# Kernel optimization log

Measured on AMD Instinct MI355X. Metric: run time of the kernel, lower is better.

## Reference

```python
import jax, jax.numpy as jnp
import numpy as np

N = 10000      # nodes
E = 160000     # edges
F_IN = 128     # input_feature
G = 64         # graphs in batch
NC = 10        # num_classes
H1, H2, H3 = 1000, 700, 200


def _xavier(k, fi, fo):
    lim = float(np.sqrt(6.0 / (fi + fo)))
    return jax.random.uniform(k, (fi, fo), jnp.float32, -lim, lim)


def setup_inputs() -> dict:
    key = jax.random.key(0)
    ks = jax.random.split(key, 8)
    x = jax.random.normal(ks[0], (N, F_IN), jnp.float32)
    edge_index = jax.random.randint(ks[1], (2, E), 0, N)
    batch = jnp.sort(jax.random.randint(ks[2], (N,), 0, G))
    return {
        "x": x,
        "edge_index": edge_index,
        "batch": batch,
        "W1": _xavier(ks[3], F_IN, H1), "b1": jnp.zeros((H1,), jnp.float32),
        "W2": _xavier(ks[4], H1, H2),   "b2": jnp.zeros((H2,), jnp.float32),
        "W3": _xavier(ks[5], H2, H3),   "b3": jnp.zeros((H3,), jnp.float32),
        "Wl": _xavier(ks[6], H3, NC),   "bl": jnp.zeros((NC,), jnp.float32),
    }


def _gcn_conv(x, W, b, src, dst, dinv):
    # GCNConv: h = xW; out_i = sum_{j->i} d_j^-1/2 d_i^-1/2 h_j + d_i^-1 h_i + b
    h = x @ W
    coef = dinv[src] * dinv[dst]                      # [E]
    agg = jax.ops.segment_sum(h[src] * coef[:, None], dst, num_segments=N)
    agg = agg + h * (dinv * dinv)[:, None]            # self-loop term
    return agg + b


def reference(x, edge_index, batch, W1, b1, W2, b2, W3, b3, Wl, bl):
    src, dst = edge_index[0], edge_index[1]
    # degree with self-loops (edge weight 1), computed on target nodes
    deg = jax.ops.segment_sum(jnp.ones((E,), x.dtype), dst, num_segments=N) + 1.0
    dinv = jax.lax.rsqrt(deg)

    h = jax.nn.relu(_gcn_conv(x, W1, b1, src, dst, dinv))
    h = jax.nn.relu(_gcn_conv(h, W2, b2, src, dst, dinv))
    h = jax.nn.relu(_gcn_conv(h, W3, b3, src, dst, dinv))

    # global_mean_pool over graph ids
    s = jax.ops.segment_sum(h, batch, num_segments=G)
    cnt = jax.ops.segment_sum(jnp.ones((N,), h.dtype), batch, num_segments=G)
    pooled = s / jnp.maximum(cnt, 1.0)[:, None]

    # dropout is identity in eval mode
    return pooled @ Wl + bl
```

## Files before the change

kernel.cpp:

```cpp
#include <hip/hip_runtime.h>
#include <hip/hip_bf16.h>
#include <stdint.h>


#define SLOT 64

__device__ __forceinline__ uint16_t f2b(float f) {
    union { float f; uint32_t u; } v; v.f = f;
    return (uint16_t)((v.u + 0x7fffu + ((v.u >> 16) & 1u)) >> 16);
}
__device__ __forceinline__ float blo(uint32_t u) { union { uint32_t u; float f; } v; v.u = u << 16; return v.f; }
__device__ __forceinline__ float bhi(uint32_t u) { union { uint32_t u; float f; } v; v.u = u & 0xffff0000u; return v.f; }

__global__ void k_prep(const float* __restrict__ W1, const float* __restrict__ W2,
                       const float* __restrict__ W3,
                       uint16_t* __restrict__ T1, uint16_t* __restrict__ T2,
                       uint16_t* __restrict__ T3,
                       const float* __restrict__ b1, const float* __restrict__ b2,
                       const float* __restrict__ b3,
                       float* __restrict__ p1, float* __restrict__ p2,
                       float* __restrict__ p3,
                       const int* __restrict__ src, const int* __restrict__ dst,
                       int* __restrict__ cursor, int* __restrict__ slots,
                       float* __restrict__ outz, int outn,
                       int E, int N, int F, int H1, int H2, int H3,
                       int Fp, int H1p, int H2p, int H3p) {
    __shared__ float tile[32][33];
    int z = blockIdx.z;
    if (z < 3) {
        const float* W; uint16_t* T; int K, Nn, Kp, Np;
        if (z == 0)      { W = W1; T = T1; K = F;  Nn = H1; Kp = Fp;  Np = H1p; }
        else if (z == 1) { W = W2; T = T2; K = H1; Nn = H2; Kp = H1p; Np = H2p; }
        else             { W = W3; T = T3; K = H2; Nn = H3; Kp = H2p; Np = H3p; }
        if ((int)blockIdx.x * 32 >= Kp || (int)blockIdx.y * 32 >= Np) return;
        int k0 = blockIdx.x * 32, n0 = blockIdx.y * 32;
        int tx = threadIdx.x, ty = threadIdx.y;
        for (int i = ty; i < 32; i += 8) {
            int k = k0 + i, n = n0 + tx;
            tile[i][tx] = (k < K && n < Nn) ? W[(size_t)k * Nn + n] : 0.f;
        }
        __syncthreads();
        for (int i = ty; i < 32; i += 8) {
            int n = n0 + i, k = k0 + tx;
            T[(size_t)n * Kp + k] = f2b(tile[tx][i]);
        }
    } else if (z == 3) {
        int id = (blockIdx.y * gridDim.x + blockIdx.x) * 256 + threadIdx.y * 32 + threadIdx.x;
        if (id < H1p) p1[id] = (id < H1) ? b1[id] : 0.f;
        else if (id < H1p + H2p) { int k = id - H1p; p2[k] = (k < H2) ? b2[k] : 0.f; }
        else if (id < H1p + H2p + H3p) { int k = id - H1p - H2p; p3[k] = (k < H3) ? b3[k] : 0.f; }
        if (id < outn) outz[id] = 0.f;
    } else {
        int fb = blockIdx.y * gridDim.x + blockIdx.x;
        int g = fb & 7, b = fb >> 3;
        int seg = (N + 7) >> 3;
        int lo = g * seg;
        int hi = lo + seg; if (hi > N) hi = N;
        int per = (E + 127) >> 7;
        int e0 = b * per;
        int e1 = e0 + per; if (e1 > E) e1 = E;
        int tid = threadIdx.y * 32 + threadIdx.x;
        for (int e = e0 + tid; e < e1; e += 256) {
            int d = dst[e];
            if (d >= lo && d < hi) {
                int s = src[e];
                int pos = atomicAdd(&cursor[d], 1);
                if (pos < SLOT) slots[d * SLOT + pos] = s;
            }
        }
    }
}

__global__ __launch_bounds__(256) void k_agg_x(
    const float* __restrict__ x, uint16_t* __restrict__ out,
    const int* __restrict__ deg_, const int* __restrict__ slots,
    int N, int F4, int pc) {
    int seg = blockIdx.x & 7;
    int segLen = (N + 7) >> 3;
    int wave = threadIdx.x >> 6, lane = threadIdx.x & 63;
    int half = lane >> 5, sub = lane & 31;
    int item = (blockIdx.x >> 3) * 128 + wave * 32 + sub;
    int rel = item / pc;
    if (rel >= segLen) return;
    int node = seg * segLen + rel;
    if (node >= N) return;
    int j = item - rel * pc;
    int degN = deg_[node];
    float dv = rsqrtf((float)degN + 1.0f);
    int deg = degN > SLOT ? SLOT : degN;
    int base = node * SLOT;
    const float4* x4 = (const float4*)x;
    float a[8] = {0.f, 0.f, 0.f, 0.f, 0.f, 0.f, 0.f, 0.f};
    if (half == 0) {
        float4 xl = x4[(size_t)node * F4 + 2 * j];
        float4 xh = x4[(size_t)node * F4 + 2 * j + 1];
        a[0] = dv * xl.x; a[1] = dv * xl.y; a[2] = dv * xl.z; a[3] = dv * xl.w;
        a[4] = dv * xh.x; a[5] = dv * xh.y; a[6] = dv * xh.z; a[7] = dv * xh.w;
    }
    int D8 = deg & ~7;
    for (int e = 4 * half; e < D8; e += 8) {
        int4 q = *(const int4*)&slots[base + e];
        float c0 = rsqrtf((float)deg_[q.x] + 1.0f);
        float c1 = rsqrtf((float)deg_[q.y] + 1.0f);
        float c2 = rsqrtf((float)deg_[q.z] + 1.0f);
        float c3 = rsqrtf((float)deg_[q.w] + 1.0f);
        float4 l0 = x4[(size_t)q.x * F4 + 2 * j], h0 = x4[(size_t)q.x * F4 + 2 * j + 1];
        float4 l1 = x4[(size_t)q.y * F4 + 2 * j], h1 = x4[(size_t)q.y * F4 + 2 * j + 1];
        float4 l2 = x4[(size_t)q.z * F4 + 2 * j], h2 = x4[(size_t)q.z * F4 + 2 * j + 1];
        float4 l3 = x4[(size_t)q.w * F4 + 2 * j], h3 = x4[(size_t)q.w * F4 + 2 * j + 1];
        a[0] += c0 * l0.x; a[1] += c0 * l0.y; a[2] += c0 * l0.z; a[3] += c0 * l0.w;
        a[4] += c0 * h0.x; a[5] += c0 * h0.y; a[6] += c0 * h0.z; a[7] += c0 * h0.w;
        a[0] += c1 * l1.x; a[1] += c1 * l1.y; a[2] += c1 * l1.z; a[3] += c1 * l1.w;
        a[4] += c1 * h1.x; a[5] += c1 * h1.y; a[6] += c1 * h1.z; a[7] += c1 * h1.w;
        a[0] += c2 * l2.x; a[1] += c2 * l2.y; a[2] += c2 * l2.z; a[3] += c2 * l2.w;
        a[4] += c2 * h2.x; a[5] += c2 * h2.y; a[6] += c2 * h2.z; a[7] += c2 * h2.w;
        a[0] += c3 * l3.x; a[1] += c3 * l3.y; a[2] += c3 * l3.z; a[3] += c3 * l3.w;
        a[4] += c3 * h3.x; a[5] += c3 * h3.y; a[6] += c3 * h3.z; a[7] += c3 * h3.w;
    }
    int t0 = half ? (D8 + 4 < deg ? D8 + 4 : deg) : D8;
    int t1 = half ? deg : (D8 + 4 < deg ? D8 + 4 : deg);
    for (int e = t0; e < t1; ++e) {
        int s = slots[base + e];
        float c = rsqrtf((float)deg_[s] + 1.0f);
        float4 l = x4[(size_t)s * F4 + 2 * j], h = x4[(size_t)s * F4 + 2 * j + 1];
        a[0] += c * l.x; a[1] += c * l.y; a[2] += c * l.z; a[3] += c * l.w;
        a[4] += c * h.x; a[5] += c * h.y; a[6] += c * h.z; a[7] += c * h.w;
    }
#pragma unroll
    for (int t = 0; t < 8; ++t) a[t] += __shfl_xor(a[t], 32, 64);
    if (half == 0) {
#pragma unroll
        for (int t = 0; t < 8; ++t) a[t] *= dv;
        uint4 o;
        o.x = (uint32_t)f2b(a[0]) | ((uint32_t)f2b(a[1]) << 16);
        o.y = (uint32_t)f2b(a[2]) | ((uint32_t)f2b(a[3]) << 16);
        o.z = (uint32_t)f2b(a[4]) | ((uint32_t)f2b(a[5]) << 16);
        o.w = (uint32_t)f2b(a[6]) | ((uint32_t)f2b(a[7]) << 16);
        ((uint4*)out)[(size_t)node * (F4 >> 1) + j] = o;
    }
}

__global__ __launch_bounds__(256) void k_agg_panel(
    const uint16_t* __restrict__ in, uint16_t* __restrict__ out,
    const int* __restrict__ deg_, const int* __restrict__ slots,
    const float* __restrict__ bias,
    int N, int Hc, int pc, int P, int relu) {
    int slotg = blockIdx.x & 7;
    int panel = slotg % P;
    int seg   = slotg / P;
    int nseg  = 8 / P;
    int segLen = (N + nseg - 1) / nseg;
    int wave = threadIdx.x >> 6, lane = threadIdx.x & 63;
    int half = lane >> 5, sub = lane & 31;
    int item = (blockIdx.x >> 3) * 128 + wave * 32 + sub;
    int rel = item / pc;
    if (rel >= segLen) return;
    int node = seg * segLen + rel;
    if (node >= N) return;
    int j = panel * pc + (item - rel * pc);
    int deg = deg_[node];
    float dv = rsqrtf((float)deg + 1.0f);
    if (deg > SLOT) deg = SLOT;
    int base = node * SLOT;
    const uint4* in4 = (const uint4*)in;
    float a[8] = {0.f, 0.f, 0.f, 0.f, 0.f, 0.f, 0.f, 0.f};
    if (half == 0) {
        uint4 v = in4[(size_t)node * Hc + j];
        a[0] = blo(v.x); a[1] = bhi(v.x);
        a[2] = blo(v.y); a[3] = bhi(v.y);
        a[4] = blo(v.z); a[5] = bhi(v.z);
        a[6] = blo(v.w); a[7] = bhi(v.w);
    }
    int D8 = deg & ~7;
    int e = 4 * half;
    if (e < D8) {
        int4 q = *(const int4*)&slots[base + e];
        uint4 h0 = in4[(size_t)q.x * Hc + j];
        uint4 h1 = in4[(size_t)q.y * Hc + j];
        uint4 h2 = in4[(size_t)q.z * Hc + j];
        uint4 h3 = in4[(size_t)q.w * Hc + j];
        for (e += 8; e < D8; e += 8) {
            int4 qn = *(const int4*)&slots[base + e];
            uint4 g0 = in4[(size_t)qn.x * Hc + j];
            uint4 g1 = in4[(size_t)qn.y * Hc + j];
            uint4 g2 = in4[(size_t)qn.z * Hc + j];
            uint4 g3 = in4[(size_t)qn.w * Hc + j];
            a[0] += blo(h0.x); a[1] += bhi(h0.x);
            a[2] += blo(h0.y); a[3] += bhi(h0.y);
            a[4] += blo(h0.z); a[5] += bhi(h0.z);
            a[6] += blo(h0.w); a[7] += bhi(h0.w);
            a[0] += blo(h1.x); a[1] += bhi(h1.x);
            a[2] += blo(h1.y); a[3] += bhi(h1.y);
            a[4] += blo(h1.z); a[5] += bhi(h1.z);
            a[6] += blo(h1.w); a[7] += bhi(h1.w);
            a[0] += blo(h2.x); a[1] += bhi(h2.x);
            a[2] += blo(h2.y); a[3] += bhi(h2.y);
            a[4] += blo(h2.z); a[5] += bhi(h2.z);
            a[6] += blo(h2.w); a[7] += bhi(h2.w);
            a[0] += blo(h3.x); a[1] += bhi(h3.x);
            a[2] += blo(h3.y); a[3] += bhi(h3.y);
            a[4] += blo(h3.z); a[5] += bhi(h3.z);
            a[6] += blo(h3.w); a[7] += bhi(h3.w);
            h0 = g0; h1 = g1; h2 = g2; h3 = g3;
        }
        a[0] += blo(h0.x); a[1] += bhi(h0.x);
        a[2] += blo(h0.y); a[3] += bhi(h0.y);
        a[4] += blo(h0.z); a[5] += bhi(h0.z);
        a[6] += blo(h0.w); a[7] += bhi(h0.w);
        a[0] += blo(h1.x); a[1] += bhi(h1.x);
        a[2] += blo(h1.y); a[3] += bhi(h1.y);
        a[4] += blo(h1.z); a[5] += bhi(h1.z);
        a[6] += blo(h1.w); a[7] += bhi(h1.w);
        a[0] += blo(h2.x); a[1] += bhi(h2.x);
        a[2] += blo(h2.y); a[3] += bhi(h2.y);
        a[4] += blo(h2.z); a[5] += bhi(h2.z);
        a[6] += blo(h2.w); a[7] += bhi(h2.w);
        a[0] += blo(h3.x); a[1] += bhi(h3.x);
        a[2] += blo(h3.y); a[3] += bhi(h3.y);
        a[4] += blo(h3.z); a[5] += bhi(h3.z);
        a[6] += blo(h3.w); a[7] += bhi(h3.w);
    }
    int t0 = half ? (D8 + 4 < deg ? D8 + 4 : deg) : D8;
    int t1 = half ? deg : (D8 + 4 < deg ? D8 + 4 : deg);
    for (int ee = t0; ee < t1; ++ee) {
        int s0 = slots[base + ee];
        uint4 h = in4[(size_t)s0 * Hc + j];
        a[0] += blo(h.x); a[1] += bhi(h.x);
        a[2] += blo(h.y); a[3] += bhi(h.y);
        a[4] += blo(h.z); a[5] += bhi(h.z);
        a[6] += blo(h.w); a[7] += bhi(h.w);
    }
#pragma unroll
    for (int t = 0; t < 8; ++t) a[t] += __shfl_xor(a[t], 32, 64);
    if (half == 0) {
        if (bias) {
            const float4* b4 = (const float4*)bias;
            float4 b0 = b4[2 * j], b1 = b4[2 * j + 1];
            a[0] = fmaf(a[0], dv, b0.x); a[1] = fmaf(a[1], dv, b0.y);
            a[2] = fmaf(a[2], dv, b0.z); a[3] = fmaf(a[3], dv, b0.w);
            a[4] = fmaf(a[4], dv, b1.x); a[5] = fmaf(a[5], dv, b1.y);
            a[6] = fmaf(a[6], dv, b1.z); a[7] = fmaf(a[7], dv, b1.w);
        } else {
#pragma unroll
            for (int t = 0; t < 8; ++t) a[t] *= dv;
        }
        if (relu) {
#pragma unroll
            for (int t = 0; t < 8; ++t) a[t] = fmaxf(a[t], 0.f);
        }
        uint4 o;
        o.x = (uint32_t)f2b(a[0]) | ((uint32_t)f2b(a[1]) << 16);
        o.y = (uint32_t)f2b(a[2]) | ((uint32_t)f2b(a[3]) << 16);
        o.z = (uint32_t)f2b(a[4]) | ((uint32_t)f2b(a[5]) << 16);
        o.w = (uint32_t)f2b(a[6]) | ((uint32_t)f2b(a[7]) << 16);
        ((uint4*)out)[(size_t)node * Hc + j] = o;
    }
}

__global__ __launch_bounds__(256) void k_pool_cls4(
    const uint16_t* __restrict__ h, const int* __restrict__ batch,
    const float* __restrict__ Wl, const float* __restrict__ bl,
    float* __restrict__ out, int N, int H, int Hc, int NC) {
    __shared__ float part[8][26][8];
    __shared__ float pooled[200];
    int g = blockIdx.x >> 2, b = blockIdx.x & 3;
    int tid = threadIdx.x;
    int lo = 0, hi = N;
    while (lo < hi) { int m = (lo + hi) >> 1; if (batch[m] < g) lo = m + 1; else hi = m; }
    int start = lo; hi = N;
    while (lo < hi) { int m = (lo + hi) >> 1; if (batch[m] < g + 1) lo = m + 1; else hi = m; }
    int end = lo;
    int j = tid & 31, s = tid >> 5;
    int jmax = H >> 3;
    const uint4* h4 = (const uint4*)h;
    if (j < jmax) {
        float a[8] = {0.f, 0.f, 0.f, 0.f, 0.f, 0.f, 0.f, 0.f};
        for (int node = start + s * 4 + b; node < end; node += 32) {
            uint4 v = h4[(size_t)node * Hc + j];
            a[0] += blo(v.x); a[1] += bhi(v.x);
            a[2] += blo(v.y); a[3] += bhi(v.y);
            a[4] += blo(v.z); a[5] += bhi(v.z);
            a[6] += blo(v.w); a[7] += bhi(v.w);
        }
#pragma unroll
        for (int t = 0; t < 8; ++t) part[s][j][t] = a[t];
    }
    __syncthreads();
    if (tid < H) {
        float sum = 0.f;
#pragma unroll
        for (int ss = 0; ss < 8; ++ss) sum += part[ss][tid >> 3][tid & 7];
        pooled[tid] = sum;
    }
    __syncthreads();
    if (tid < 64) {
        float scale = 1.0f / fmaxf((float)(end - start), 1.0f);
        int c = tid & 15, q = tid >> 4;
        float acc = 0.f;
        if (c < NC) {
            for (int k = q; k < H; k += 4)
                acc += pooled[k] * Wl[(size_t)k * NC + c];
        }
        acc += __shfl_xor(acc, 16, 64);
        acc += __shfl_xor(acc, 32, 64);
        if (q == 0 && c < NC) {
            float v = acc * scale;
            if (b == 0) v += bl[c];
            atomicAdd(&out[(size_t)g * NC + c], v);
        }
    }
}

typedef __attribute__((ext_vector_type(8))) short short8;
typedef __attribute__((ext_vector_type(4))) float floatx4;

#define LDSP(p) ((__attribute__((address_space(3))) void*)(uintptr_t)(p))
#define GLBP(p) ((const __attribute__((address_space(1))) void*)(uintptr_t)(p))

__global__ __launch_bounds__(256) void k_gemm128(
    const uint16_t* __restrict__ A, const uint16_t* __restrict__ Bt,
    const float* __restrict__ bias, uint16_t* __restrict__ Cout,
    int M, int Kp, int Np, int relu, int nrg, int nr,
    const int* __restrict__ degp) {
    int bid = blockIdx.x;
    int rsub = bid & 7;
    int t_ = bid >> 3;
    int rg = t_ % nrg, cc = t_ / nrg;
    int rt = rg * 8 + rsub;
    if (rt >= nr) return;
    int row0 = rt * 128, col0 = cc * 128;

    __shared__ uint16_t As[128 * 64];
    __shared__ uint16_t Bs[128 * 64];
    int tid = threadIdx.x;
    int wave = tid >> 6, lane = tid & 63;
    int quad = lane >> 4, m16 = lane & 15;
    int wr = wave >> 1, wc = wave & 1;

    int rA = tid >> 3;
    int cA = (tid & 7) ^ (rA & 7);
    const uint16_t* gA = A  + (size_t)(row0 + rA) * Kp + cA * 8;
    const uint16_t* gB = Bt + (size_t)(col0 + rA) * Kp + cA * 8;
    uint16_t* lA = As + tid * 8;
    uint16_t* lB = Bs + tid * 8;
    size_t rowStep32 = (size_t)32 * Kp;

    floatx4 acc[4][4];
#pragma unroll
    for (int i = 0; i < 4; ++i)
#pragma unroll
        for (int j = 0; j < 4; ++j) acc[i][j] = (floatx4){0.f, 0.f, 0.f, 0.f};

    const short* Ash = (const short*)As;
    const short* Bsh = (const short*)Bs;
    int swA = m16 & 7;

    for (int k0 = 0; k0 < Kp; k0 += 64) {
#pragma unroll
        for (int p = 0; p < 4; ++p) {
            __builtin_amdgcn_global_load_lds(GLBP(gA + p * rowStep32), LDSP(lA + p * 2048), 16, 0, 0);
            __builtin_amdgcn_global_load_lds(GLBP(gB + p * rowStep32), LDSP(lB + p * 2048), 16, 0, 0);
        }
        gA += 64; gB += 64;
        __syncthreads();
#pragma unroll
        for (int h = 0; h < 2; ++h) {
            short8 af[4], bf[4];
            int c = h * 4 + quad;
            int pos = (c ^ swA) * 8;
#pragma unroll
            for (int i = 0; i < 4; ++i)
                af[i] = *(const short8*)&Ash[(wr * 64 + i * 16 + m16) * 64 + pos];
#pragma unroll
            for (int j = 0; j < 4; ++j)
                bf[j] = *(const short8*)&Bsh[(wc * 64 + j * 16 + m16) * 64 + pos];
#pragma unroll
            for (int i = 0; i < 4; ++i)
#pragma unroll
                for (int j = 0; j < 4; ++j)
                    acc[i][j] = __builtin_amdgcn_mfma_f32_16x16x32_bf16(af[i], bf[j], acc[i][j], 0, 0, 0);
        }
        __syncthreads();
    }

    float bv[4];
#pragma unroll
    for (int j = 0; j < 4; ++j) {
        int n = col0 + wc * 64 + j * 16 + m16;
        bv[j] = bias ? bias[n] : 0.f;
    }
#pragma unroll
    for (int i = 0; i < 4; ++i) {
        int mBase = row0 + wr * 64 + i * 16 + quad * 4;
#pragma unroll
        for (int r = 0; r < 4; ++r) {
            int m = mBase + r;
            if (m < M) {
                float s = degp ? rsqrtf((float)degp[m] + 1.0f) : 1.f;
#pragma unroll
                for (int j = 0; j < 4; ++j) {
                    int n = col0 + wc * 64 + j * 16 + m16;
                    float v = acc[i][j][r] * s + bv[j];
                    if (relu) v = fmaxf(v, 0.f);
                    Cout[(size_t)m * Np + n] = f2b(v);
                }
            }
        }
    }
}

__global__ __launch_bounds__(256) void k_gemm64(
    const uint16_t* __restrict__ A, const uint16_t* __restrict__ Bt,
    const float* __restrict__ bias, uint16_t* __restrict__ Cout,
    int M, int Kp, int Np, int relu, int nrg, int nr,
    const int* __restrict__ degp) {
    int bid = blockIdx.x;
    int rsub = bid & 7;
    int t_ = bid >> 3;
    int rg = t_ % nrg, cc = t_ / nrg;
    int rt = rg * 8 + rsub;
    if (rt >= nr) return;
    int row0 = rt * 128, col0 = cc * 64;

    __shared__ uint16_t As[128 * 64];
    __shared__ uint16_t Bs[64 * 64];
    int tid = threadIdx.x;
    int wave = tid >> 6, lane = tid & 63;
    int quad = lane >> 4, m16 = lane & 15;
    int wr = wave >> 1, wc = wave & 1;

    int rA = tid >> 3;
    int cA = (tid & 7) ^ (rA & 7);
    const uint16_t* gA = A  + (size_t)(row0 + rA) * Kp + cA * 8;
    const uint16_t* gB = Bt + (size_t)(col0 + rA) * Kp + cA * 8;
    uint16_t* lA = As + tid * 8;
    uint16_t* lB = Bs + tid * 8;
    size_t rowStep32 = (size_t)32 * Kp;

    floatx4 acc[4][2];
#pragma unroll
    for (int i = 0; i < 4; ++i)
#pragma unroll
        for (int j = 0; j < 2; ++j) acc[i][j] = (floatx4){0.f, 0.f, 0.f, 0.f};

    const short* Ash = (const short*)As;
    const short* Bsh = (const short*)Bs;
    int swA = m16 & 7;

    for (int k0 = 0; k0 < Kp; k0 += 64) {
#pragma unroll
        for (int p = 0; p < 4; ++p)
            __builtin_amdgcn_global_load_lds(GLBP(gA + p * rowStep32), LDSP(lA + p * 2048), 16, 0, 0);
#pragma unroll
        for (int p = 0; p < 2; ++p)
            __builtin_amdgcn_global_load_lds(GLBP(gB + p * rowStep32), LDSP(lB + p * 2048), 16, 0, 0);
        gA += 64; gB += 64;
        __syncthreads();
#pragma unroll
        for (int h = 0; h < 2; ++h) {
            short8 af[4], bf[2];
            int c = h * 4 + quad;
            int pos = (c ^ swA) * 8;
#pragma unroll
            for (int i = 0; i < 4; ++i)
                af[i] = *(const short8*)&Ash[(wr * 64 + i * 16 + m16) * 64 + pos];
#pragma unroll
            for (int j = 0; j < 2; ++j)
                bf[j] = *(const short8*)&Bsh[(wc * 32 + j * 16 + m16) * 64 + pos];
#pragma unroll
            for (int i = 0; i < 4; ++i)
#pragma unroll
                for (int j = 0; j < 2; ++j)
                    acc[i][j] = __builtin_amdgcn_mfma_f32_16x16x32_bf16(af[i], bf[j], acc[i][j], 0, 0, 0);
        }
        __syncthreads();
    }

    float bv[2];
#pragma unroll
    for (int j = 0; j < 2; ++j) {
        int n = col0 + wc * 32 + j * 16 + m16;
        bv[j] = bias ? bias[n] : 0.f;
    }
#pragma unroll
    for (int i = 0; i < 4; ++i) {
        int mBase = row0 + wr * 64 + i * 16 + quad * 4;
#pragma unroll
        for (int r = 0; r < 4; ++r) {
            int m = mBase + r;
            if (m < M) {
                float s = degp ? rsqrtf((float)degp[m] + 1.0f) : 1.f;
#pragma unroll
                for (int j = 0; j < 2; ++j) {
                    int n = col0 + wc * 32 + j * 16 + m16;
                    float v = acc[i][j][r] * s + bv[j];
                    if (relu) v = fmaxf(v, 0.f);
                    Cout[(size_t)m * Np + n] = f2b(v);
                }
            }
        }
    }
}

static inline size_t align256(size_t x) { return (x + 255) & ~(size_t)255; }
static inline int pad128(int x) { return (x + 127) & ~127; }

extern "C" void kernel_launch(void* const* d_in, const int* in_sizes, int n_in,
                              void* d_out, int out_size, void* d_ws, size_t ws_size,
                              hipStream_t stream) {
    const float* x   = (const float*)d_in[0];
    const int*   ei  = (const int*)d_in[1];
    const int*   bat = (const int*)d_in[2];
    const float* W1  = (const float*)d_in[3];
    const float* b1  = (const float*)d_in[4];
    const float* W2  = (const float*)d_in[5];
    const float* b2  = (const float*)d_in[6];
    const float* W3  = (const float*)d_in[7];
    const float* b3  = (const float*)d_in[8];
    const float* Wl  = (const float*)d_in[9];
    const float* bl  = (const float*)d_in[10];

    const int N  = in_sizes[2];
    const int E  = in_sizes[1] / 2;
    const int F  = in_sizes[0] / N;
    const int H1 = in_sizes[4];
    const int H2 = in_sizes[6];
    const int H3 = in_sizes[8];
    const int NC = in_sizes[10];
    const int* src = ei;
    const int* dst = ei + E;

    const int Mp  = pad128(N);
    const int Fp  = F;
    const int H1p = pad128(H1);
    const int H2p = pad128(H2);
    const int H3p = pad128(H3);

    char* p = (char*)d_ws;
    size_t off = 0;
    auto carve = [&](size_t bytes) { void* q = p + off; off += align256(bytes); return q; };
    uint16_t* bufA   = (uint16_t*)carve((size_t)Mp * 2048);
    uint16_t* bufB   = (uint16_t*)carve((size_t)Mp * 2048);
    uint16_t* W1t    = (uint16_t*)carve((size_t)H1p * Fp * 2);
    uint16_t* W2t    = (uint16_t*)carve((size_t)H2p * H1p * 2);
    uint16_t* W3t    = (uint16_t*)carve((size_t)H3p * H2p * 2);
    float* b1p       = (float*)carve((size_t)H1p * 4);
    float* b2p       = (float*)carve((size_t)H2p * 4);
    float* b3p       = (float*)carve((size_t)H3p * 4);
    int*   cursor    = (int*)carve((size_t)N * 4);
    int*   slots     = (int*)carve((size_t)N * SLOT * 4);
    (void)ws_size;

    hipMemsetAsync(cursor, 0, (size_t)N * 4, stream);

    k_prep<<<dim3(32, 32, 5), dim3(32, 8), 0, stream>>>(
        W1, W2, W3, W1t, W2t, W3t, b1, b2, b3, b1p, b2p, b3p,
        src, dst, cursor, slots, (float*)d_out, out_size,
        E, N, F, H1, H2, H3, Fp, H1p, H2p, H3p);

    auto agg_grid = [&](int P, int pc) {
        int nseg = 8 / P;
        int segLen = (N + nseg - 1) / nseg;
        return 8 * ((segLen * pc + 127) / 128);
    };

    const int nr  = Mp / 128;
    const int nrg = (nr + 7) / 8;

    k_agg_x<<<agg_grid(1, F / 8), 256, 0, stream>>>(
        x, bufA, cursor, slots, N, F / 4, F / 8);
    k_gemm128<<<nrg * 8 * (H1p / 128), 256, 0, stream>>>(
        bufA, W1t, b1p, bufB, N, Fp, H1p, 1, nrg, nr, nullptr);

    k_gemm128<<<nrg * 8 * (H2p / 128), 256, 0, stream>>>(
        bufB, W2t, nullptr, bufA, N, H1p, H2p, 0, nrg, nr, cursor);
    k_agg_panel<<<agg_grid(8, 11), 256, 0, stream>>>(
        bufA, bufB, cursor, slots, b2p, N, 96, 11, 8, 1);

    k_gemm64<<<nrg * 8 * (H3p / 64), 256, 0, stream>>>(
        bufB, W3t, nullptr, bufA, N, H2p, H3p, 0, nrg, nr, cursor);
    k_agg_panel<<<agg_grid(4, 7), 256, 0, stream>>>(
        bufA, bufB, cursor, slots, b3p, N, 32, 7, 4, 1);

    k_pool_cls4<<<64 * 4, 256, 0, stream>>>(
        (const uint16_t*)bufB, bat, Wl, bl, (float*)d_out, N, H3, H3p >> 3, NC);
}
```

Baseline: 226.4 us.

## Build edge slots with shared-memory cursors, pre-cast x to bf16, pipeline gather loop

The edge-binning stage now uses 64 blocks, each owning a node range and counting in shared-memory cursors before writing them to global memory. This removes the separate memset and the global atomics, but every block now scans the full dst array. The input features are converted to bf16 inside the prep kernel, so the first aggregation gathers half as many bytes. The aggregation loop is also software-pipelined so the next neighbor rows load while the current ones accumulate. The full-array scan per block may make the binning stage long-latency and limit its parallelism.

```diff
diff --git a/kernel.cpp b/kernel.cpp
--- a/kernel.cpp
+++ b/kernel.cpp
@@ -20,12 +20,14 @@
                        const float* __restrict__ b3,
                        float* __restrict__ p1, float* __restrict__ p2,
                        float* __restrict__ p3,
+                       const float* __restrict__ x, uint16_t* __restrict__ xbu,
                        const int* __restrict__ src, const int* __restrict__ dst,
                        int* __restrict__ cursor, int* __restrict__ slots,
                        float* __restrict__ outz, int outn,
                        int E, int N, int F, int H1, int H2, int H3,
-                       int Fp, int H1p, int H2p, int H3p) {
+                       int Fp, int H1p, int H2p, int H3p, int n8) {
     __shared__ float tile[32][33];
+    __shared__ int lcur[160];
     int z = blockIdx.z;
     if (z < 3) {
         const float* W; uint16_t* T; int K, Nn, Kp, Np;
@@ -50,31 +52,64 @@
         else if (id < H1p + H2p) { int k = id - H1p; p2[k] = (k < H2) ? b2[k] : 0.f; }
         else if (id < H1p + H2p + H3p) { int k = id - H1p - H2p; p3[k] = (k < H3) ? b3[k] : 0.f; }
         if (id < outn) outz[id] = 0.f;
+        if (id < n8) {
+            const float4* x4 = (const float4*)x;
+            float4 a = x4[2 * id], b = x4[2 * id + 1];
+            uint4 o;
+            o.x = (uint32_t)f2b(a.x) | ((uint32_t)f2b(a.y) << 16);
+            o.y = (uint32_t)f2b(a.z) | ((uint32_t)f2b(a.w) << 16);
+            o.z = (uint32_t)f2b(b.x) | ((uint32_t)f2b(b.y) << 16);
+            o.w = (uint32_t)f2b(b.z) | ((uint32_t)f2b(b.w) << 16);
+            ((uint4*)xbu)[id] = o;
+        }
     } else {
         int fb = blockIdx.y * gridDim.x + blockIdx.x;
-        int g = fb & 7, b = fb >> 3;
-        int seg = (N + 7) >> 3;
-        int lo = g * seg;
+        if (fb >= 64) return;
+        int seg = (N + 63) >> 6;
+        int lo = fb * seg;
         int hi = lo + seg; if (hi > N) hi = N;
-        int per = (E + 127) >> 7;
-        int e0 = b * per;
-        int e1 = e0 + per; if (e1 > E) e1 = E;
         int tid = threadIdx.y * 32 + threadIdx.x;
-        for (int e = e0 + tid; e < e1; e += 256) {
+        for (int i = tid; i < seg; i += 256) lcur[i] = 0;
+        __syncthreads();
+        const int4* dst4 = (const int4*)dst;
+        int E4 = E >> 2;
+        for (int i = tid; i < E4; i += 256) {
+            int4 d4 = dst4[i];
+            int e = 4 * i;
+            if (d4.x >= lo && d4.x < hi) {
+                int pos = atomicAdd(&lcur[d4.x - lo], 1);
+                if (pos < SLOT) slots[d4.x * SLOT + pos] = src[e];
+            }
+            if (d4.y >= lo && d4.y < hi) {
+                int pos = atomicAdd(&lcur[d4.y - lo], 1);
+                if (pos < SLOT) slots[d4.y * SLOT + pos] = src[e + 1];
+            }
+            if (d4.z >= lo && d4.z < hi) {
+                int pos = atomicAdd(&lcur[d4.z - lo], 1);
+                if (pos < SLOT) slots[d4.z * SLOT + pos] = src[e + 2];
+            }
+            if (d4.w >= lo && d4.w < hi) {
+                int pos = atomicAdd(&lcur[d4.w - lo], 1);
+                if (pos < SLOT) slots[d4.w * SLOT + pos] = src[e + 3];
+            }
+        }
+        for (int e = (E4 << 2) + tid; e < E; e += 256) {
             int d = dst[e];
             if (d >= lo && d < hi) {
-                int s = src[e];
-                int pos = atomicAdd(&cursor[d], 1);
-                if (pos < SLOT) slots[d * SLOT + pos] = s;
+                int pos = atomicAdd(&lcur[d - lo], 1);
+                if (pos < SLOT) slots[d * SLOT + pos] = src[e];
             }
         }
+        __syncthreads();
+        for (int i = tid; i < seg; i += 256)
+            if (lo + i < N) cursor[lo + i] = lcur[i];
     }
 }
 
 __global__ __launch_bounds__(256) void k_agg_x(
-    const float* __restrict__ x, uint16_t* __restrict__ out,
+    const uint16_t* __restrict__ in, uint16_t* __restrict__ out,
     const int* __restrict__ deg_, const int* __restrict__ slots,
-    int N, int F4, int pc) {
+    int N, int Hc, int pc) {
     int seg = blockIdx.x & 7;
     int segLen = (N + 7) >> 3;
     int wave = threadIdx.x >> 6, lane = threadIdx.x & 63;
@@ -89,42 +124,83 @@
     float dv = rsqrtf((float)degN + 1.0f);
     int deg = degN > SLOT ? SLOT : degN;
     int base = node * SLOT;
-    const float4* x4 = (const float4*)x;
+    const uint4* in4 = (const uint4*)in;
     float a[8] = {0.f, 0.f, 0.f, 0.f, 0.f, 0.f, 0.f, 0.f};
     if (half == 0) {
-        float4 xl = x4[(size_t)node * F4 + 2 * j];
-        float4 xh = x4[(size_t)node * F4 + 2 * j + 1];
-        a[0] = dv * xl.x; a[1] = dv * xl.y; a[2] = dv * xl.z; a[3] = dv * xl.w;
-        a[4] = dv * xh.x; a[5] = dv * xh.y; a[6] = dv * xh.z; a[7] = dv * xh.w;
+        uint4 v = in4[(size_t)node * Hc + j];
+        a[0] = dv * blo(v.x); a[1] = dv * bhi(v.x);
+        a[2] = dv * blo(v.y); a[3] = dv * bhi(v.y);
+        a[4] = dv * blo(v.z); a[5] = dv * bhi(v.z);
+        a[6] = dv * blo(v.w); a[7] = dv * bhi(v.w);
     }
     int D8 = deg & ~7;
-    for (int e = 4 * half; e < D8; e += 8) {
+    int e = 4 * half;
+    if (e < D8) {
         int4 q = *(const int4*)&slots[base + e];
+        uint4 h0 = in4[(size_t)q.x * Hc + j];
+        uint4 h1 = in4[(size_t)q.y * Hc + j];
+        uint4 h2 = in4[(size_t)q.z * Hc + j];
+        uint4 h3 = in4[(size_t)q.w * Hc + j];
         float c0 = rsqrtf((float)deg_[q.x] + 1.0f);
         float c1 = rsqrtf((float)deg_[q.y] + 1.0f);
         float c2 = rsqrtf((float)deg_[q.z] + 1.0f);
         float c3 = rsqrtf((float)deg_[q.w] + 1.0f);
-        float4 l0 = x4[(size_t)q.x * F4 + 2 * j], h0 = x4[(size_t)q.x * F4 + 2 * j + 1];
-        float4 l1 = x4[(size_t)q.y * F4 + 2 * j], h1 = x4[(size_t)q.y * F4 + 2 * j + 1];
-        float4 l2 = x4[(size_t)q.z * F4 + 2 * j], h2 = x4[(size_t)q.z * F4 + 2 * j + 1];
-        float4 l3 = x4[(size_t)q.w * F4 + 2 * j], h3 = x4[(size_t)q.w * F4 + 2 * j + 1];
-        a[0] += c0 * l0.x; a[1] += c0 * l0.y; a[2] += c0 * l0.z; a[3] += c0 * l0.w;
-        a[4] += c0 * h0.x; a[5] += c0 * h0.y; a[6] += c0 * h0.z; a[7] += c0 * h0.w;
-        a[0] += c1 * l1.x; a[1] += c1 * l1.y; a[2] += c1 * l1.z; a[3] += c1 * l1.w;
-        a[4] += c1 * h1.x; a[5] += c1 * h1.y; a[6] += c1 * h1.z; a[7] += c1 * h1.w;
-        a[0] += c2 * l2.x; a[1] += c2 * l2.y; a[2] += c2 * l2.z; a[3] += c2 * l2.w;
-        a[4] += c2 * h2.x; a[5] += c2 * h2.y; a[6] += c2 * h2.z; a[7] += c2 * h2.w;
-        a[0] += c3 * l3.x; a[1] += c3 * l3.y; a[2] += c3 * l3.z; a[3] += c3 * l3.w;
-        a[4] += c3 * h3.x; a[5] += c3 * h3.y; a[6] += c3 * h3.z; a[7] += c3 * h3.w;
+        for (e += 8; e < D8; e += 8) {
+            int4 qn = *(const int4*)&slots[base + e];
+            uint4 g0 = in4[(size_t)qn.x * Hc + j];
+            uint4 g1 = in4[(size_t)qn.y * Hc + j];
+            uint4 g2 = in4[(size_t)qn.z * Hc + j];
+            uint4 g3 = in4[(size_t)qn.w * Hc + j];
+            float d0 = rsqrtf((float)deg_[qn.x] + 1.0f);
+            float d1 = rsqrtf((float)deg_[qn.y] + 1.0f);
+            float d2 = rsqrtf((float)deg_[qn.z] + 1.0f);
+            float d3 = rsqrtf((float)deg_[qn.w] + 1.0f);
+            a[0] += c0 * blo(h0.x); a[1] += c0 * bhi(h0.x);
+            a[2] += c0 * blo(h0.y); a[3] += c0 * bhi(h0.y);
+            a[4] += c0 * blo(h0.z); a[5] += c0 * bhi(h0.z);
+            a[6] += c0 * blo(h0.w); a[7] += c0 * bhi(h0.w);
+            a[0] += c1 * blo(h1.x); a[1] += c1 * bhi(h1.x);
+            a[2] += c1 * blo(h1.y); a[3] += c1 * bhi(h1.y);
+            a[4] += c1 * blo(h1.z); a[5] += c1 * bhi(h1.z);
+            a[6] += c1 * blo(h1.w); a[7] += c1 * bhi(h1.w);
+            a[0] += c2 * blo(h2.x); a[1] += c2 * bhi(h2.x);
+            a[2] += c2 * blo(h2.y); a[3] += c2 * bhi(h2.y);
+            a[4] += c2 * blo(h2.z); a[5] += c2 * bhi(h2.z);
+            a[6] += c2 * blo(h2.w); a[7] += c2 * bhi(h2.w);
+            a[0] += c3 * blo(h3.x); a[1] += c3 * bhi(h3.x);
+            a[2] += c3 * blo(h3.y); a[3] += c3 * bhi(h3.y);
+            a[4] += c3 * blo(h3.z); a[5] += c3 * bhi(h3.z);
+            a[6] += c3 * blo(h3.w); a[7] += c3 * bhi(h3.w);
+            h0 = g0; h1 = g1; h2 = g2; h3 = g3;
+            c0 = d0; c1 = d1; c2 = d2; c3 = d3;
+        }
+        a[0] += c0 * blo(h0.x); a[1] += c0 * bhi(h0.x);
+        a[2] += c0 * blo(h0.y); a[3] += c0 * bhi(h0.y);
+        a[4] += c0 * blo(h0.z); a[5] += c0 * bhi(h0.z);
+        a[6] += c0 * blo(h0.w); a[7] += c0 * bhi(h0.w);
+        a[0] += c1 * blo(h1.x); a[1] += c1 * bhi(h1.x);
+        a[2] += c1 * blo(h1.y); a[3] += c1 * bhi(h1.y);
+        a[4] += c1 * blo(h1.z); a[5] += c1 * bhi(h1.z);
+        a[6] += c1 * blo(h1.w); a[7] += c1 * bhi(h1.w);
+        a[0] += c2 * blo(h2.x); a[1] += c2 * bhi(h2.x);
+        a[2] += c2 * blo(h2.y); a[3] += c2 * bhi(h2.y);
+        a[4] += c2 * blo(h2.z); a[5] += c2 * bhi(h2.z);
+        a[6] += c2 * blo(h2.w); a[7] += c2 * bhi(h2.w);
+        a[0] += c3 * blo(h3.x); a[1] += c3 * bhi(h3.x);
+        a[2] += c3 * blo(h3.y); a[3] += c3 * bhi(h3.y);
+        a[4] += c3 * blo(h3.z); a[5] += c3 * bhi(h3.z);
+        a[6] += c3 * blo(h3.w); a[7] += c3 * bhi(h3.w);
     }
     int t0 = half ? (D8 + 4 < deg ? D8 + 4 : deg) : D8;
     int t1 = half ? deg : (D8 + 4 < deg ? D8 + 4 : deg);
-    for (int e = t0; e < t1; ++e) {
-        int s = slots[base + e];
+    for (int ee = t0; ee < t1; ++ee) {
+        int s = slots[base + ee];
         float c = rsqrtf((float)deg_[s] + 1.0f);
-        float4 l = x4[(size_t)s * F4 + 2 * j], h = x4[(size_t)s * F4 + 2 * j + 1];
-        a[0] += c * l.x; a[1] += c * l.y; a[2] += c * l.z; a[3] += c * l.w;
-        a[4] += c * h.x; a[5] += c * h.y; a[6] += c * h.z; a[7] += c * h.w;
+        uint4 h = in4[(size_t)s * Hc + j];
+        a[0] += c * blo(h.x); a[1] += c * bhi(h.x);
+        a[2] += c * blo(h.y); a[3] += c * bhi(h.y);
+        a[4] += c * blo(h.z); a[5] += c * bhi(h.z);
+        a[6] += c * blo(h.w); a[7] += c * bhi(h.w);
     }
 #pragma unroll
     for (int t = 0; t < 8; ++t) a[t] += __shfl_xor(a[t], 32, 64);
@@ -136,7 +212,7 @@
         o.y = (uint32_t)f2b(a[2]) | ((uint32_t)f2b(a[3]) << 16);
         o.z = (uint32_t)f2b(a[4]) | ((uint32_t)f2b(a[5]) << 16);
         o.w = (uint32_t)f2b(a[6]) | ((uint32_t)f2b(a[7]) << 16);
-        ((uint4*)out)[(size_t)node * (F4 >> 1) + j] = o;
+        ((uint4*)out)[(size_t)node * Hc + j] = o;
     }
 }
 
@@ -539,6 +615,7 @@
     char* p = (char*)d_ws;
     size_t off = 0;
     auto carve = [&](size_t bytes) { void* q = p + off; off += align256(bytes); return q; };
+    uint16_t* xbu    = (uint16_t*)carve((size_t)Mp * Fp * 2);
     uint16_t* bufA   = (uint16_t*)carve((size_t)Mp * 2048);
     uint16_t* bufB   = (uint16_t*)carve((size_t)Mp * 2048);
     uint16_t* W1t    = (uint16_t*)carve((size_t)H1p * Fp * 2);
@@ -551,12 +628,10 @@
     int*   slots     = (int*)carve((size_t)N * SLOT * 4);
     (void)ws_size;
 
-    hipMemsetAsync(cursor, 0, (size_t)N * 4, stream);
-
     k_prep<<<dim3(32, 32, 5), dim3(32, 8), 0, stream>>>(
         W1, W2, W3, W1t, W2t, W3t, b1, b2, b3, b1p, b2p, b3p,
-        src, dst, cursor, slots, (float*)d_out, out_size,
-        E, N, F, H1, H2, H3, Fp, H1p, H2p, H3p);
+        x, xbu, src, dst, cursor, slots, (float*)d_out, out_size,
+        E, N, F, H1, H2, H3, Fp, H1p, H2p, H3p, N * F / 8);
 
     auto agg_grid = [&](int P, int pc) {
         int nseg = 8 / P;
@@ -568,7 +643,7 @@
     const int nrg = (nr + 7) / 8;
 
     k_agg_x<<<agg_grid(1, F / 8), 256, 0, stream>>>(
-        x, bufA, cursor, slots, N, F / 4, F / 8);
+        xbu, bufA, cursor, slots, N, F / 8, F / 8);
     k_gemm128<<<nrg * 8 * (H1p / 128), 256, 0, stream>>>(
         bufA, W1t, b1p, bufB, N, Fp, H1p, 1, nrg, nr, nullptr);
 
```

Result: slower. 342.0 us (+51.1%).
